# Performance work log

Hardware: AMD Instinct MI355X
Metric: run time of the kernel (lower is better)

The kernel has to match this reference:

```python
import jax, jax.numpy as jnp
import numpy as np

N_NODES = 100000   # num_nodes_ori
N_EDGES = 1600000  # avg degree 16
D_IN = 128
D_OUT = 128


def setup_inputs() -> dict:
    key = jax.random.key(0)
    k_x, k_w, k_r, k_c, k_v = jax.random.split(key, 5)
    stdv = 1.0 / np.sqrt(D_OUT).astype(np.float32)
    X = jax.random.normal(k_x, (N_NODES, D_IN), dtype=jnp.float32)
    weights = jax.random.uniform(k_w, (D_IN, D_OUT), jnp.float32, -stdv, stdv)
    # CSR-equivalent edge list of the normalized adjacency A (values = norm coeffs)
    edge_rows = jnp.sort(jax.random.randint(k_r, (N_EDGES,), 0, N_NODES, dtype=jnp.int32))
    edge_cols = jax.random.randint(k_c, (N_EDGES,), 0, N_NODES, dtype=jnp.int32)
    edge_vals = jax.random.uniform(k_v, (N_EDGES,), jnp.float32)
    return {"X": X, "weights": weights, "edge_rows": edge_rows,
            "edge_cols": edge_cols, "edge_vals": edge_vals}


def reference(X, weights, edge_rows, edge_cols, edge_vals):
    # Dense feature transform: X' = X @ W   [N, D_OUT]
    XW = jnp.matmul(X, weights)
    # Sparse aggregation out = A @ X' (edge-list SpMM, same math as Libra6SpMM):
    # gather source features, scale by edge value, scatter-add into dst rows.
    msgs = XW[edge_cols] * edge_vals[:, None]            # [E, D_OUT]
    out = jax.ops.segment_sum(msgs, edge_rows, num_segments=N_NODES)
    return out
```

## Files before the change

kernel.cpp:

```cpp
#include <hip/hip_runtime.h>

#define D 128

typedef __attribute__((ext_vector_type(8))) short bf16x8;
typedef __attribute__((ext_vector_type(4))) float f32x4;

__device__ __forceinline__ ushort f2bf(float f) {
    unsigned u = __float_as_uint(f);
    u += 0x7fffu + ((u >> 16) & 1u);
    return (ushort)(u >> 16);
}
__device__ __forceinline__ float bf2f(ushort h) {
    return __uint_as_float(((unsigned)h) << 16);
}

__global__ __launch_bounds__(256) void convert_wt(const float* __restrict__ W,
                                                  ushort* __restrict__ Wt) {
    int idx = blockIdx.x * 256 + threadIdx.x;
    int c = idx >> 7, k = idx & 127;
    Wt[c * D + k] = f2bf(W[k * D + c]);
}

__global__ __launch_bounds__(256) void build_rowptr(const int* __restrict__ rows,
                                                    int E, int* __restrict__ rp,
                                                    int N) {
    int r = blockIdx.x * 256 + threadIdx.x;
    if (r > N) return;
    int lo = 0, hi = E;
    while (lo < hi) {
        int mid = (lo + hi) >> 1;
        if (rows[mid] < r) lo = mid + 1; else hi = mid;
    }
    rp[r] = lo;
}

__global__ __launch_bounds__(256) void gemm_mfma(const float* __restrict__ X,
                                                 const ushort* __restrict__ Wt,
                                                 ushort* __restrict__ XW, int M) {
    __shared__ ushort Wl[D][D + 8];

    const int t = threadIdx.x;
#pragma unroll
    for (int p = 0; p < 8; ++p) {
        int idx = p * 256 + t;
        int row = idx >> 4, ch = idx & 15;
        *(uint4*)&Wl[row][ch * 8] = *(const uint4*)&Wt[row * D + ch * 8];
    }
    __syncthreads();

    const int lane = t & 63, wid = t >> 6;
    const int r0 = blockIdx.x * 64 + wid * 16;

    int arow = r0 + (lane & 15);
    if (arow >= M) arow = M - 1;
    const float* xp = X + (size_t)arow * D + ((lane >> 4) * 8);

    bf16x8 a[4];
#pragma unroll
    for (int ks = 0; ks < 4; ++ks) {
        float4 f0 = *(const float4*)(xp + ks * 32);
        float4 f1 = *(const float4*)(xp + ks * 32 + 4);
        bf16x8 av;
        av[0] = (short)f2bf(f0.x); av[1] = (short)f2bf(f0.y);
        av[2] = (short)f2bf(f0.z); av[3] = (short)f2bf(f0.w);
        av[4] = (short)f2bf(f1.x); av[5] = (short)f2bf(f1.y);
        av[6] = (short)f2bf(f1.z); av[7] = (short)f2bf(f1.w);
        a[ks] = av;
    }

    f32x4 acc[8];
#pragma unroll
    for (int jt = 0; jt < 8; ++jt) acc[jt] = (f32x4){0.f, 0.f, 0.f, 0.f};

#pragma unroll
    for (int jt = 0; jt < 8; ++jt) {
        const ushort* bp = &Wl[jt * 16 + (lane & 15)][(lane >> 4) * 8];
#pragma unroll
        for (int ks = 0; ks < 4; ++ks) {
            bf16x8 b = *(const bf16x8*)(bp + ks * 32);
            acc[jt] = __builtin_amdgcn_mfma_f32_16x16x32_bf16(a[ks], b, acc[jt],
                                                              0, 0, 0);
        }
    }

#pragma unroll
    for (int jt = 0; jt < 8; ++jt) {
#pragma unroll
        for (int q = 0; q < 4; ++q) {
            int rr = r0 + (lane >> 4) * 4 + q;
            if (rr < M)
                XW[(size_t)rr * D + jt * 16 + (lane & 15)] = f2bf(acc[jt][q]);
        }
    }
}

__global__ __launch_bounds__(256) void spmm_csr(const ushort* __restrict__ XW,
                                                const int* __restrict__ rp,
                                                const int* __restrict__ cols,
                                                const float* __restrict__ vals,
                                                float* __restrict__ out, int N) {
    const int lane = threadIdx.x & 63;
    const int r = blockIdx.x * 4 + (threadIdx.x >> 6);
    if (r >= N) return;

    const int s = rp[r], e = rp[r + 1];
    const uint* base = (const uint*)XW;
    float ax = 0.f, ay = 0.f;

    int i = s;
    for (; i + 1 < e; i += 2) {
        int   c0 = cols[i],     c1 = cols[i + 1];
        float v0 = vals[i],     v1 = vals[i + 1];
        uint  u0 = base[(size_t)c0 * 64 + lane];
        uint  u1 = base[(size_t)c1 * 64 + lane];
        ax += v0 * bf2f((ushort)(u0 & 0xffff));
        ay += v0 * bf2f((ushort)(u0 >> 16));
        ax += v1 * bf2f((ushort)(u1 & 0xffff));
        ay += v1 * bf2f((ushort)(u1 >> 16));
    }
    if (i < e) {
        int   c = cols[i];
        float v = vals[i];
        uint  u = base[(size_t)c * 64 + lane];
        ax += v * bf2f((ushort)(u & 0xffff));
        ay += v * bf2f((ushort)(u >> 16));
    }
    ((float2*)out)[(size_t)r * 64 + lane] = make_float2(ax, ay);
}

extern "C" void kernel_launch(void* const* d_in, const int* in_sizes, int n_in,
                              void* d_out, int out_size, void* d_ws, size_t ws_size,
                              hipStream_t stream) {
    const float* X    = (const float*)d_in[0];
    const float* W    = (const float*)d_in[1];
    const int*   rows = (const int*)d_in[2];
    const int*   cols = (const int*)d_in[3];
    const float* vals = (const float*)d_in[4];
    float*       out  = (float*)d_out;

    const int M = in_sizes[0] / D;
    const int E = in_sizes[2];

    char* ws = (char*)d_ws;
    ushort* XWb = (ushort*)ws;
    int*    rp  = (int*)(ws + (size_t)M * D * sizeof(ushort));
    ushort* Wt  = (ushort*)(ws + (size_t)M * D * sizeof(ushort)
                               + (((size_t)(M + 1) * sizeof(int) + 15) & ~(size_t)15));

    convert_wt  <<<64, 256, 0, stream>>>(W, Wt);
    build_rowptr<<<(M + 256) / 256, 256, 0, stream>>>(rows, E, rp, M);
    gemm_mfma   <<<(M + 63) / 64, 256, 0, stream>>>(X, Wt, XWb, M);
    spmm_csr    <<<(M + 3) / 4, 256, 0, stream>>>(XWb, rp, cols, vals, out, M);
}
```

Before: 230.1 us.

## Prepack weights in MFMA fragment order, drop LDS staging, unroll SpMM gather by four

The weight conversion kernel now writes W in the exact per-lane MFMA fragment order, so the GEMM loads B fragments straight from global memory (L2-resident) instead of staging W into shared memory behind a barrier. Swapping the MFMA operand order transposes the accumulator layout, so each lane can write packed 32-bit pairs of bf16 outputs along a row rather than scattered 16-bit stores. The SpMM inner loop is unrolled to four edges to keep more independent gathers in flight. The risks are more global-load traffic for W per wave, and extra register pressure in the SpMM.

```diff
diff --git a/kernel.cpp b/kernel.cpp
--- a/kernel.cpp
+++ b/kernel.cpp
@@ -14,11 +14,16 @@
     return __uint_as_float(((unsigned)h) << 16);
 }
 
-__global__ __launch_bounds__(256) void convert_wt(const float* __restrict__ W,
-                                                  ushort* __restrict__ Wt) {
+__global__ __launch_bounds__(256) void convert_wf(const float* __restrict__ W,
+                                                  ushort* __restrict__ Wf) {
     int idx = blockIdx.x * 256 + threadIdx.x;
-    int c = idx >> 7, k = idx & 127;
-    Wt[c * D + k] = f2bf(W[k * D + c]);
+    int j    = idx & 7;
+    int lane = (idx >> 3) & 63;
+    int f    = idx >> 9;
+    int jt = f >> 2, ks = f & 3;
+    int col = jt * 16 + (lane & 15);
+    int k   = ks * 32 + ((lane >> 4) * 8) + j;
+    Wf[idx] = f2bf(W[k * D + col]);
 }
 
 __global__ __launch_bounds__(256) void build_rowptr(const int* __restrict__ rows,
@@ -35,27 +40,16 @@
 }
 
 __global__ __launch_bounds__(256) void gemm_mfma(const float* __restrict__ X,
-                                                 const ushort* __restrict__ Wt,
+                                                 const ushort* __restrict__ Wf,
                                                  ushort* __restrict__ XW, int M) {
-    __shared__ ushort Wl[D][D + 8];
-
-    const int t = threadIdx.x;
-#pragma unroll
-    for (int p = 0; p < 8; ++p) {
-        int idx = p * 256 + t;
-        int row = idx >> 4, ch = idx & 15;
-        *(uint4*)&Wl[row][ch * 8] = *(const uint4*)&Wt[row * D + ch * 8];
-    }
-    __syncthreads();
-
-    const int lane = t & 63, wid = t >> 6;
+    const int t = threadIdx.x, lane = t & 63, wid = t >> 6;
     const int r0 = blockIdx.x * 64 + wid * 16;
 
     int arow = r0 + (lane & 15);
     if (arow >= M) arow = M - 1;
     const float* xp = X + (size_t)arow * D + ((lane >> 4) * 8);
 
-    bf16x8 a[4];
+    bf16x8 xf[4];
 #pragma unroll
     for (int ks = 0; ks < 4; ++ks) {
         float4 f0 = *(const float4*)(xp + ks * 32);
@@ -65,31 +59,33 @@
         av[2] = (short)f2bf(f0.z); av[3] = (short)f2bf(f0.w);
         av[4] = (short)f2bf(f1.x); av[5] = (short)f2bf(f1.y);
         av[6] = (short)f2bf(f1.z); av[7] = (short)f2bf(f1.w);
-        a[ks] = av;
+        xf[ks] = av;
     }
+
+    const bf16x8* wf = (const bf16x8*)Wf + lane;
 
     f32x4 acc[8];
 #pragma unroll
     for (int jt = 0; jt < 8; ++jt) acc[jt] = (f32x4){0.f, 0.f, 0.f, 0.f};
 
 #pragma unroll
-    for (int jt = 0; jt < 8; ++jt) {
-        const ushort* bp = &Wl[jt * 16 + (lane & 15)][(lane >> 4) * 8];
+    for (int jt = 0; jt < 8; ++jt)
 #pragma unroll
         for (int ks = 0; ks < 4; ++ks) {
-            bf16x8 b = *(const bf16x8*)(bp + ks * 32);
-            acc[jt] = __builtin_amdgcn_mfma_f32_16x16x32_bf16(a[ks], b, acc[jt],
-                                                              0, 0, 0);
+            bf16x8 w = wf[(jt * 4 + ks) * 64];
+            acc[jt] = __builtin_amdgcn_mfma_f32_16x16x32_bf16(w, xf[ks],
+                                                              acc[jt], 0, 0, 0);
         }
-    }
 
+    const int row = r0 + (lane & 15);
+    if (row < M) {
+        uint* dst = (uint*)(XW + (size_t)row * D + (lane >> 4) * 4);
 #pragma unroll
-    for (int jt = 0; jt < 8; ++jt) {
-#pragma unroll
-        for (int q = 0; q < 4; ++q) {
-            int rr = r0 + (lane >> 4) * 4 + q;
-            if (rr < M)
-                XW[(size_t)rr * D + jt * 16 + (lane & 15)] = f2bf(acc[jt][q]);
+        for (int jt = 0; jt < 8; ++jt) {
+            uint lo = (uint)f2bf(acc[jt][0]) | ((uint)f2bf(acc[jt][1]) << 16);
+            uint hi = (uint)f2bf(acc[jt][2]) | ((uint)f2bf(acc[jt][3]) << 16);
+            uint* p = dst + jt * 8;
+            p[0] = lo; p[1] = hi;
         }
     }
 }
@@ -108,17 +104,25 @@
     float ax = 0.f, ay = 0.f;
 
     int i = s;
-    for (; i + 1 < e; i += 2) {
+    for (; i + 3 < e; i += 4) {
         int   c0 = cols[i],     c1 = cols[i + 1];
+        int   c2 = cols[i + 2], c3 = cols[i + 3];
         float v0 = vals[i],     v1 = vals[i + 1];
+        float v2 = vals[i + 2], v3 = vals[i + 3];
         uint  u0 = base[(size_t)c0 * 64 + lane];
         uint  u1 = base[(size_t)c1 * 64 + lane];
+        uint  u2 = base[(size_t)c2 * 64 + lane];
+        uint  u3 = base[(size_t)c3 * 64 + lane];
         ax += v0 * bf2f((ushort)(u0 & 0xffff));
         ay += v0 * bf2f((ushort)(u0 >> 16));
         ax += v1 * bf2f((ushort)(u1 & 0xffff));
         ay += v1 * bf2f((ushort)(u1 >> 16));
+        ax += v2 * bf2f((ushort)(u2 & 0xffff));
+        ay += v2 * bf2f((ushort)(u2 >> 16));
+        ax += v3 * bf2f((ushort)(u3 & 0xffff));
+        ay += v3 * bf2f((ushort)(u3 >> 16));
     }
-    if (i < e) {
+    for (; i < e; ++i) {
         int   c = cols[i];
         float v = vals[i];
         uint  u = base[(size_t)c * 64 + lane];
@@ -144,11 +148,11 @@
     char* ws = (char*)d_ws;
     ushort* XWb = (ushort*)ws;
     int*    rp  = (int*)(ws + (size_t)M * D * sizeof(ushort));
-    ushort* Wt  = (ushort*)(ws + (size_t)M * D * sizeof(ushort)
+    ushort* Wf  = (ushort*)(ws + (size_t)M * D * sizeof(ushort)
                                + (((size_t)(M + 1) * sizeof(int) + 15) & ~(size_t)15));
 
-    convert_wt  <<<64, 256, 0, stream>>>(W, Wt);
+    convert_wf  <<<64, 256, 0, stream>>>(W, Wf);
     build_rowptr<<<(M + 256) / 256, 256, 0, stream>>>(rows, E, rp, M);
-    gemm_mfma   <<<(M + 63) / 64, 256, 0, stream>>>(X, Wt, XWb, M);
+    gemm_mfma   <<<(M + 63) / 64, 256, 0, stream>>>(X, Wf, XWb, M);
     spmm_csr    <<<(M + 3) / 4, 256, 0, stream>>>(XWb, rp, cols, vals, out, M);
 }
```

Measured after the change: 209.5 us. -9.0%, faster.

## Fuse weight conversion and rowptr search into GEMM and SpMM kernels, batch gathers

Applied to the files above, without the earlier changes.

Removes the separate weight-transpose and row-pointer kernels. Each GEMM block now converts W to bf16 itself into an MFMA-friendly LDS layout, and the operands are swapped so results store as packed pairs. Each SpMM wavefront binary-searches its own row bounds using two lanes. The SpMM loop now issues 8 gathers at a time with predicated tails and uses nontemporal output stores. The cost is redundant per-block W conversion and per-row binary searches over the full edge array, traded for two fewer launches and more memory-level parallelism.

```diff
diff --git a/kernel.cpp b/kernel.cpp
--- a/kernel.cpp
+++ b/kernel.cpp
@@ -4,6 +4,8 @@
 
 typedef __attribute__((ext_vector_type(8))) short bf16x8;
 typedef __attribute__((ext_vector_type(4))) float f32x4;
+typedef __attribute__((ext_vector_type(2))) float f32x2;
+typedef __attribute__((ext_vector_type(2))) uint  u32x2;
 
 __device__ __forceinline__ ushort f2bf(float f) {
     unsigned u = __float_as_uint(f);
@@ -14,39 +16,32 @@
     return __uint_as_float(((unsigned)h) << 16);
 }
 
-__global__ __launch_bounds__(256) void convert_wt(const float* __restrict__ W,
-                                                  ushort* __restrict__ Wt) {
-    int idx = blockIdx.x * 256 + threadIdx.x;
-    int c = idx >> 7, k = idx & 127;
-    Wt[c * D + k] = f2bf(W[k * D + c]);
-}
-
-__global__ __launch_bounds__(256) void build_rowptr(const int* __restrict__ rows,
-                                                    int E, int* __restrict__ rp,
-                                                    int N) {
-    int r = blockIdx.x * 256 + threadIdx.x;
-    if (r > N) return;
-    int lo = 0, hi = E;
-    while (lo < hi) {
-        int mid = (lo + hi) >> 1;
-        if (rows[mid] < r) lo = mid + 1; else hi = mid;
-    }
-    rp[r] = lo;
-}
-
 __global__ __launch_bounds__(256) void gemm_mfma(const float* __restrict__ X,
-                                                 const ushort* __restrict__ Wt,
+                                                 const float* __restrict__ W,
                                                  ushort* __restrict__ XW, int M) {
-    __shared__ ushort Wl[D][D + 8];
+    __shared__ ushort Wl[16384];
 
     const int t = threadIdx.x;
+    {
+        const int c = t & 127, half = t >> 7;
+        const int jt = c >> 4;
 #pragma unroll
-    for (int p = 0; p < 8; ++p) {
-        int idx = p * 256 + t;
-        int row = idx >> 4, ch = idx & 15;
-        *(uint4*)&Wl[row][ch * 8] = *(const uint4*)&Wt[row * D + ch * 8];
+        for (int g = 0; g < 8; ++g) {
+            const int k8   = half + g * 2;
+            const int ks   = k8 >> 2;
+            const int lsub = (k8 & 3) * 16 + (c & 15);
+            uint4 pk;
+            ushort tmp[8];
+#pragma unroll
+            for (int j = 0; j < 8; ++j)
+                tmp[j] = f2bf(W[(k8 * 8 + j) * D + c]);
+            pk.x = (uint)tmp[0] | ((uint)tmp[1] << 16);
+            pk.y = (uint)tmp[2] | ((uint)tmp[3] << 16);
+            pk.z = (uint)tmp[4] | ((uint)tmp[5] << 16);
+            pk.w = (uint)tmp[6] | ((uint)tmp[7] << 16);
+            *(uint4*)&Wl[(((jt * 4 + ks) * 64) + lsub) * 8] = pk;
+        }
     }
-    __syncthreads();
 
     const int lane = t & 63, wid = t >> 6;
     const int r0 = blockIdx.x * 64 + wid * 16;
@@ -55,7 +50,7 @@
     if (arow >= M) arow = M - 1;
     const float* xp = X + (size_t)arow * D + ((lane >> 4) * 8);
 
-    bf16x8 a[4];
+    bf16x8 xf[4];
 #pragma unroll
     for (int ks = 0; ks < 4; ++ks) {
         float4 f0 = *(const float4*)(xp + ks * 32);
@@ -65,67 +60,81 @@
         av[2] = (short)f2bf(f0.z); av[3] = (short)f2bf(f0.w);
         av[4] = (short)f2bf(f1.x); av[5] = (short)f2bf(f1.y);
         av[6] = (short)f2bf(f1.z); av[7] = (short)f2bf(f1.w);
-        a[ks] = av;
+        xf[ks] = av;
     }
+
+    __syncthreads();
+
+    const bf16x8* wl = (const bf16x8*)Wl + lane;
 
     f32x4 acc[8];
 #pragma unroll
     for (int jt = 0; jt < 8; ++jt) acc[jt] = (f32x4){0.f, 0.f, 0.f, 0.f};
 
 #pragma unroll
-    for (int jt = 0; jt < 8; ++jt) {
-        const ushort* bp = &Wl[jt * 16 + (lane & 15)][(lane >> 4) * 8];
+    for (int jt = 0; jt < 8; ++jt)
 #pragma unroll
         for (int ks = 0; ks < 4; ++ks) {
-            bf16x8 b = *(const bf16x8*)(bp + ks * 32);
-            acc[jt] = __builtin_amdgcn_mfma_f32_16x16x32_bf16(a[ks], b, acc[jt],
-                                                              0, 0, 0);
+            bf16x8 w = wl[(jt * 4 + ks) * 64];
+            acc[jt] = __builtin_amdgcn_mfma_f32_16x16x32_bf16(w, xf[ks],
+                                                              acc[jt], 0, 0, 0);
         }
-    }
 
+    const int row = r0 + (lane & 15);
+    if (row < M) {
+        uint* dst = (uint*)XW + (size_t)row * 64 + (lane >> 4) * 2;
 #pragma unroll
-    for (int jt = 0; jt < 8; ++jt) {
-#pragma unroll
-        for (int q = 0; q < 4; ++q) {
-            int rr = r0 + (lane >> 4) * 4 + q;
-            if (rr < M)
-                XW[(size_t)rr * D + jt * 16 + (lane & 15)] = f2bf(acc[jt][q]);
+        for (int jt = 0; jt < 8; ++jt) {
+            u32x2 pv;
+            pv[0] = (uint)f2bf(acc[jt][0]) | ((uint)f2bf(acc[jt][1]) << 16);
+            pv[1] = (uint)f2bf(acc[jt][2]) | ((uint)f2bf(acc[jt][3]) << 16);
+            *(u32x2*)(dst + jt * 8) = pv;
         }
     }
 }
 
 __global__ __launch_bounds__(256) void spmm_csr(const ushort* __restrict__ XW,
-                                                const int* __restrict__ rp,
+                                                const int* __restrict__ rows,
                                                 const int* __restrict__ cols,
                                                 const float* __restrict__ vals,
-                                                float* __restrict__ out, int N) {
+                                                float* __restrict__ out,
+                                                int N, int E) {
     const int lane = threadIdx.x & 63;
     const int r = blockIdx.x * 4 + (threadIdx.x >> 6);
     if (r >= N) return;
 
-    const int s = rp[r], e = rp[r + 1];
+    int tgt = r + (lane != 0);
+    int lo = 0, hi = E;
+    while (lo < hi) {
+        int mid = (lo + hi) >> 1;
+        if (rows[mid] < tgt) lo = mid + 1; else hi = mid;
+    }
+    const int s = __shfl(lo, 0);
+    const int e = __shfl(lo, 1);
+
     const uint* base = (const uint*)XW;
     float ax = 0.f, ay = 0.f;
 
-    int i = s;
-    for (; i + 1 < e; i += 2) {
-        int   c0 = cols[i],     c1 = cols[i + 1];
-        float v0 = vals[i],     v1 = vals[i + 1];
-        uint  u0 = base[(size_t)c0 * 64 + lane];
-        uint  u1 = base[(size_t)c1 * 64 + lane];
-        ax += v0 * bf2f((ushort)(u0 & 0xffff));
-        ay += v0 * bf2f((ushort)(u0 >> 16));
-        ax += v1 * bf2f((ushort)(u1 & 0xffff));
-        ay += v1 * bf2f((ushort)(u1 >> 16));
+    for (int i = s; i < e; i += 8) {
+        int c[8]; float v[8]; uint u[8];
+#pragma unroll
+        for (int q = 0; q < 8; ++q) {
+            int idx = i + q;
+            int ci  = idx < e ? idx : e - 1;
+            c[q] = cols[ci];
+            v[q] = idx < e ? vals[ci] : 0.f;
+        }
+#pragma unroll
+        for (int q = 0; q < 8; ++q)
+            u[q] = base[(size_t)c[q] * 64 + lane];
+#pragma unroll
+        for (int q = 0; q < 8; ++q) {
+            ax += v[q] * bf2f((ushort)(u[q] & 0xffff));
+            ay += v[q] * bf2f((ushort)(u[q] >> 16));
+        }
     }
-    if (i < e) {
-        int   c = cols[i];
-        float v = vals[i];
-        uint  u = base[(size_t)c * 64 + lane];
-        ax += v * bf2f((ushort)(u & 0xffff));
-        ay += v * bf2f((ushort)(u >> 16));
-    }
-    ((float2*)out)[(size_t)r * 64 + lane] = make_float2(ax, ay);
+    f32x2 o; o[0] = ax; o[1] = ay;
+    __builtin_nontemporal_store(o, (f32x2*)out + (size_t)r * 64 + lane);
 }
 
 extern "C" void kernel_launch(void* const* d_in, const int* in_sizes, int n_in,
@@ -141,14 +150,8 @@
     const int M = in_sizes[0] / D;
     const int E = in_sizes[2];
 
-    char* ws = (char*)d_ws;
-    ushort* XWb = (ushort*)ws;
-    int*    rp  = (int*)(ws + (size_t)M * D * sizeof(ushort));
-    ushort* Wt  = (ushort*)(ws + (size_t)M * D * sizeof(ushort)
-                               + (((size_t)(M + 1) * sizeof(int) + 15) & ~(size_t)15));
+    ushort* XWb = (ushort*)d_ws;
 
-    convert_wt  <<<64, 256, 0, stream>>>(W, Wt);
-    build_rowptr<<<(M + 256) / 256, 256, 0, stream>>>(rows, E, rp, M);
-    gemm_mfma   <<<(M + 63) / 64, 256, 0, stream>>>(X, Wt, XWb, M);
-    spmm_csr    <<<(M + 3) / 4, 256, 0, stream>>>(XWb, rp, cols, vals, out, M);
+    gemm_mfma<<<(M + 63) / 64, 256, 0, stream>>>(X, W, XWb, M);
+    spmm_csr <<<(M + 3) / 4, 256, 0, stream>>>(XWb, rows, cols, vals, out, M, E);
 }
```

After: 264.4 us. 1.15x slower.
